# Performance work log

Measured on AMD Instinct MI355X. Metric: run time of the kernel, lower is better.

The kernel has to match this reference:

```python
import jax, jax.numpy as jnp
import numpy as np
import math

B, S, D = 1, 2048, 2048
H, HD, KV = 16, 128, 1
E, F, TOPK = 8, 4096, 2
EPS = 1e-5


def setup_inputs() -> dict:
    key = jax.random.key(0)
    ks = jax.random.split(key, 14)
    sc = 0.02
    inp = {
        "x": jax.random.normal(ks[0], (B, S, D), dtype=jnp.float32),
        "wq": jax.random.normal(ks[1], (D, H * HD), dtype=jnp.float32) * sc,
        "wk": jax.random.normal(ks[2], (D, KV * HD), dtype=jnp.float32) * sc,
        "wv": jax.random.normal(ks[3], (D, KV * HD), dtype=jnp.float32) * sc,
        "wo": jax.random.normal(ks[4], (H * HD, D), dtype=jnp.float32) * sc,
        "w_router": jax.random.normal(ks[5], (D, E), dtype=jnp.float32) * sc,
        "w1": jax.random.normal(ks[6], (E, D, F), dtype=jnp.float32) * sc,
        "w3": jax.random.normal(ks[7], (E, D, F), dtype=jnp.float32) * sc,
        "w2": jax.random.normal(ks[8], (E, F, D), dtype=jnp.float32) * sc,
        "s_pre_mqa": jnp.ones((D,), dtype=jnp.float32),
        "s_post_mqa": jnp.ones((D,), dtype=jnp.float32),
        "s_pre_moe": jnp.ones((D,), dtype=jnp.float32),
        "s_post_moe": jnp.ones((D,), dtype=jnp.float32),
    }
    return inp


def _rmsnorm(x, scale):
    ms = jnp.mean(x * x, axis=-1, keepdims=True)
    return x * jax.lax.rsqrt(ms + EPS) * scale


def _mqa(h, wq, wk, wv, wo):
    b, s, _ = h.shape
    q = (h @ wq).reshape(b, s, H, HD)
    k = (h @ wk).reshape(b, s, KV, HD)
    v = (h @ wv).reshape(b, s, KV, HD)
    # repeat_interleave kv heads up to H (MQA)
    k = jnp.repeat(k, H // KV, axis=2)
    v = jnp.repeat(v, H // KV, axis=2)
    scale = 1.0 / math.sqrt(HD)
    scores = jnp.einsum("bqhd,bkhd->bhqk", q, k) * scale  # [B,H,S,S]
    causal = jnp.tril(jnp.ones((s, s), dtype=bool))
    scores = jnp.where(causal, scores, jnp.float32(-jnp.inf))
    attn = jax.nn.softmax(scores, axis=-1)
    out = jnp.einsum("bhqk,bkhd->bqhd", attn, v).reshape(b, s, H * HD)
    return out @ wo


def _moe(h, w_router, w1, w2, w3):
    logits = h @ w_router                        # [B,S,E]
    probs = jax.nn.softmax(logits, axis=-1)
    topv, topi = jax.lax.top_k(probs, TOPK)      # [B,S,K]
    topv = topv / jnp.sum(topv, axis=-1, keepdims=True)
    # combine weights per expert: [B,S,E]
    combine = jnp.sum(jax.nn.one_hot(topi, E, dtype=h.dtype) * topv[..., None], axis=-2)
    out = jnp.zeros_like(h)
    for e in range(E):  # fixed small expert count
        ye = (jax.nn.silu(h @ w1[e]) * (h @ w3[e])) @ w2[e]
        out = out + combine[..., e:e + 1] * ye
    return out, combine


def reference(x, wq, wk, wv, wo, w_router, w1, w2, w3,
              s_pre_mqa, s_post_mqa, s_pre_moe, s_post_moe):
    mqa_out = _mqa(_rmsnorm(x, s_pre_mqa), wq, wk, wv, wo)
    x = x + _rmsnorm(mqa_out, s_post_mqa)  # dropout p=0 (eval)
    moe_out, router_mask = _moe(_rmsnorm(x, s_pre_moe), w_router, w1, w2, w3)
    x = x + _rmsnorm(moe_out, s_post_moe)
    return x, router_mask
```

## Files before the change

### kernel.cpp

```cpp
#include <hip/hip_runtime.h>

#define S_LEN 2048
#define DM 2048
#define NHEAD 16
#define HDIM 128
#define NEXP 8
#define FF 4096
#define EPSV 1e-5f

typedef unsigned short u16;
typedef short bf16x8 __attribute__((ext_vector_type(8)));
typedef float f32x4 __attribute__((ext_vector_type(4)));

__device__ __forceinline__ f32x4 mfma16(bf16x8 a, bf16x8 b, f32x4 c) {
  return __builtin_amdgcn_mfma_f32_16x16x32_bf16(a, b, c, 0, 0, 0);
}

__device__ __forceinline__ float bf2f(u16 u) {
  union { unsigned int i; float f; } v; v.i = ((unsigned int)u) << 16; return v.f;
}
__device__ __forceinline__ u16 f2bf(float f) {
  union { float f; unsigned int i; } v; v.f = f;
  unsigned int u = v.i;
  return (u16)((u + 0x7fffu + ((u >> 16) & 1u)) >> 16);
}

__device__ __forceinline__ void gload_lds16(const u16* g, u16* l) {
  __builtin_amdgcn_global_load_lds(
      (const __attribute__((address_space(1))) unsigned int*)(unsigned long long)g,
      (__attribute__((address_space(3))) unsigned int*)(unsigned long long)l, 16, 0, 0);
}

__device__ __forceinline__ float blocksum(float v, float* sh) {
#pragma unroll
  for (int off = 32; off; off >>= 1) v += __shfl_xor(v, off, 64);
  const int w = threadIdx.x >> 6;
  if ((threadIdx.x & 63) == 0) sh[w] = v;
  __syncthreads();
  v = sh[0] + sh[1] + sh[2] + sh[3];
  __syncthreads();
  return v;
}

__device__ __forceinline__ void convsplit_body(char* lds, const float* __restrict__ src,
                                               int ld, u16* __restrict__ dhi,
                                               u16* __restrict__ dlo, int nblk, int kblk) {
  float(*tile)[65] = reinterpret_cast<float(*)[65]>(lds);
  const int n0 = nblk * 64, k0 = kblk * 64;
  const int t = threadIdx.x;
  {
    int r = t >> 4, c4 = (t & 15) * 4;
#pragma unroll
    for (int i = 0; i < 4; ++i) {
      float4 v = *reinterpret_cast<const float4*>(src + (size_t)(k0 + r + i * 16) * ld + n0 + c4);
      tile[r + i * 16][c4 + 0] = v.x;
      tile[r + i * 16][c4 + 1] = v.y;
      tile[r + i * 16][c4 + 2] = v.z;
      tile[r + i * 16][c4 + 3] = v.w;
    }
  }
  __syncthreads();
#pragma unroll
  for (int i = 0; i < 2; ++i) {
    int idx = i * 256 + t;
    int n = idx >> 3, kc = (idx & 7) * 8;
    bf16x8 hi, lo;
#pragma unroll
    for (int j = 0; j < 8; ++j) {
      float f = tile[kc + j][n];
      u16 hv = f2bf(f);
      hi[j] = (short)hv;
      lo[j] = (short)f2bf(f - bf2f(hv));
    }
    size_t o = (size_t)(n0 + n) * 2048 + k0 + kc;
    *reinterpret_cast<bf16x8*>(dhi + o) = hi;
    *reinterpret_cast<bf16x8*>(dlo + o) = lo;
  }
}

__device__ __forceinline__ void convT_body(char* lds, const float* __restrict__ src,
                                           int R, int C, u16* __restrict__ dst,
                                           int nblk, int rblk, int e) {
  float(*tile)[65] = reinterpret_cast<float(*)[65]>(lds);
  const int n0 = nblk * 64, r0 = rblk * 64;
  const size_t bofs = (size_t)e * R * C;
  const int t = threadIdx.x;
  {
    int r = t >> 4, c4 = (t & 15) * 4;
#pragma unroll
    for (int i = 0; i < 4; ++i) {
      float4 v = *reinterpret_cast<const float4*>(src + bofs + (size_t)(r0 + r + i * 16) * C + n0 + c4);
      tile[r + i * 16][c4 + 0] = v.x;
      tile[r + i * 16][c4 + 1] = v.y;
      tile[r + i * 16][c4 + 2] = v.z;
      tile[r + i * 16][c4 + 3] = v.w;
    }
  }
  __syncthreads();
#pragma unroll
  for (int i = 0; i < 2; ++i) {
    int idx = i * 256 + t;
    int n = idx >> 3, kc = (idx & 7) * 8;
    bf16x8 pk;
#pragma unroll
    for (int j = 0; j < 8; ++j) pk[j] = (short)f2bf(tile[kc + j][n]);
    *reinterpret_cast<bf16x8*>(dst + bofs + (size_t)(n0 + n) * R + r0 + kc) = pk;
  }
}

__device__ __forceinline__ void convT_body512(char* lds, const float* __restrict__ src,
                                              int R, int C, u16* __restrict__ dst,
                                              int nblk, int rblk, int e) {
  float(*tile)[65] = reinterpret_cast<float(*)[65]>(lds);
  const int n0 = nblk * 64, r0 = rblk * 64;
  const size_t bofs = (size_t)e * R * C;
  const int t = threadIdx.x;
#pragma unroll
  for (int i = 0; i < 2; ++i) {
    int p = i * 512 + t;
    int r = p >> 4, c4 = (p & 15) * 4;
    float4 v = *reinterpret_cast<const float4*>(src + bofs + (size_t)(r0 + r) * C + n0 + c4);
    tile[r][c4 + 0] = v.x;
    tile[r][c4 + 1] = v.y;
    tile[r][c4 + 2] = v.z;
    tile[r][c4 + 3] = v.w;
  }
  __syncthreads();
  {
    int n = t >> 3, kc = (t & 7) * 8;
    bf16x8 pk;
#pragma unroll
    for (int j = 0; j < 8; ++j) pk[j] = (short)f2bf(tile[kc + j][n]);
    *reinterpret_cast<bf16x8*>(dst + bofs + (size_t)(n0 + n) * R + r0 + kc) = pk;
  }
}

__device__ __forceinline__ void rms_pre_body(char* lds, const float* __restrict__ x,
                                             const float* __restrict__ s,
                                             u16* __restrict__ h1, int row) {
  float* sh = (float*)lds;
  const int t = threadIdx.x;
  const float* xr = x + (size_t)row * DM + t * 8;
  float4 a = *reinterpret_cast<const float4*>(xr);
  float4 b = *reinterpret_cast<const float4*>(xr + 4);
  float v[8] = {a.x, a.y, a.z, a.w, b.x, b.y, b.z, b.w};
  float ss = 0.f;
#pragma unroll
  for (int j = 0; j < 8; ++j) ss += v[j] * v[j];
  float inv = rsqrtf(blocksum(ss, sh) * (1.f / DM) + EPSV);
  const float* sp = s + t * 8;
  bf16x8 hi, lo;
#pragma unroll
  for (int j = 0; j < 8; ++j) {
    float val = v[j] * inv * sp[j];
    u16 hv = f2bf(val);
    hi[j] = (short)hv;
    lo[j] = (short)f2bf(val - bf2f(hv));
  }
  *reinterpret_cast<bf16x8*>(h1 + (size_t)row * 4096 + t * 8) = hi;
  *reinterpret_cast<bf16x8*>(h1 + (size_t)row * 4096 + 2048 + t * 8) = lo;
}

__global__ __launch_bounds__(256) void fat_pre(
    const float* __restrict__ x, const float* __restrict__ spre, u16* __restrict__ h1,
    const float* __restrict__ wq, const float* __restrict__ wk, const float* __restrict__ wv,
    u16* __restrict__ BtqHi, u16* __restrict__ BtqLo) {
  __shared__ alignas(16) char lds[16640];
  int bid = blockIdx.x;
  if (bid < 2048) {
    rms_pre_body(lds, x, spre, h1, bid);
  } else if (bid < 3072) {
    int c = bid - 2048;
    convsplit_body(lds, wq, 2048, BtqHi, BtqLo, c & 31, c >> 5);
  } else if (bid < 3136) {
    int c = bid - 3072;
    convsplit_body(lds, wk, 128, BtqHi + (size_t)2048 * 2048, BtqLo + (size_t)2048 * 2048,
                   c & 1, c >> 1);
  } else {
    int c = bid - 3136;
    convsplit_body(lds, wv, 128, BtqHi + (size_t)2176 * 2048, BtqLo + (size_t)2176 * 2048,
                   c & 1, c >> 1);
  }
}

__device__ __forceinline__ void gemm3_body(
    char* lds, const u16* __restrict__ A, const u16* __restrict__ Bthi,
    const u16* __restrict__ Btlo, void* __restrict__ out,
    int mblk, int nblk, int mode, int ldc, int lo_off) {
  const int m0 = mblk * 128, n0 = nblk * 64;
  const int t = threadIdx.x, lane = t & 63, w = t >> 6;
  const int wm = (w >> 1) * 64, wn = (w & 1) * 32;
  const int l15 = lane & 15, lg = lane >> 4;
  const int wbase = t & ~63;

  u16* Ah = (u16*)lds;
  u16* Al = (u16*)(lds + 16384);
  u16* Bh = (u16*)(lds + 32768);
  u16* Bl = (u16*)(lds + 40960);

  const u16* Abh = A + (size_t)m0 * 4096;
  const u16* Abl = Abh + 2048;
  const u16* Bbh = Bthi + (size_t)n0 * 2048;
  const u16* Bbl = Btlo + (size_t)n0 * 2048;

  f32x4 acc[4][2];
#pragma unroll
  for (int m = 0; m < 4; ++m)
#pragma unroll
    for (int n = 0; n < 2; ++n) acc[m][n] = (f32x4){0.f, 0.f, 0.f, 0.f};

  for (int k0 = 0; k0 < 2048; k0 += 64) {
    __syncthreads();
#pragma unroll
    for (int i = 0; i < 4; ++i) {
      int p = i * 256 + t;
      int row = p >> 3;
      int csrc = (p & 7) ^ (row & 7);
      gload_lds16(Abh + (size_t)row * 4096 + k0 + csrc * 8, Ah + (i * 256 + wbase) * 8);
      gload_lds16(Abl + (size_t)row * 4096 + k0 + csrc * 8, Al + (i * 256 + wbase) * 8);
    }
#pragma unroll
    for (int i = 0; i < 2; ++i) {
      int p = i * 256 + t;
      int row = p >> 3;
      int csrc = (p & 7) ^ (row & 7);
      gload_lds16(Bbh + (size_t)row * 2048 + k0 + csrc * 8, Bh + (i * 256 + wbase) * 8);
      gload_lds16(Bbl + (size_t)row * 2048 + k0 + csrc * 8, Bl + (i * 256 + wbase) * 8);
    }
    __syncthreads();
#pragma unroll
    for (int kk = 0; kk < 2; ++kk) {
      bf16x8 ah[4], al[4], bh[2], bl[2];
#pragma unroll
      for (int m = 0; m < 4; ++m) {
        int row = wm + m * 16 + l15;
        int byte = row * 128 + (((kk * 4 + lg) * 16) ^ ((row & 7) << 4));
        ah[m] = *reinterpret_cast<const bf16x8*>((const char*)Ah + byte);
        al[m] = *reinterpret_cast<const bf16x8*>((const char*)Al + byte);
      }
#pragma unroll
      for (int n = 0; n < 2; ++n) {
        int row = wn + n * 16 + l15;
        int byte = row * 128 + (((kk * 4 + lg) * 16) ^ ((row & 7) << 4));
        bh[n] = *reinterpret_cast<const bf16x8*>((const char*)Bh + byte);
        bl[n] = *reinterpret_cast<const bf16x8*>((const char*)Bl + byte);
      }
#pragma unroll
      for (int m = 0; m < 4; ++m)
#pragma unroll
        for (int n = 0; n < 2; ++n) {
          acc[m][n] = mfma16(ah[m], bh[n], acc[m][n]);
          acc[m][n] = mfma16(al[m], bh[n], acc[m][n]);
          acc[m][n] = mfma16(ah[m], bl[n], acc[m][n]);
        }
    }
  }
#pragma unroll
  for (int m = 0; m < 4; ++m)
#pragma unroll
    for (int n = 0; n < 2; ++n)
#pragma unroll
      for (int r = 0; r < 4; ++r) {
        int row = m0 + wm + m * 16 + lg * 4 + r;
        int col = n0 + wn + n * 16 + l15;
        float v = acc[m][n][r];
        if (mode == 1) {
          u16* C = (u16*)out;
          u16 hv = f2bf(v);
          C[(size_t)row * ldc + col] = hv;
          C[(size_t)row * ldc + lo_off + col] = f2bf(v - bf2f(hv));
        } else {
          ((float*)out)[(size_t)row * ldc + col] = v;
        }
      }
}

__global__ __launch_bounds__(256) void gemm3_kernel(
    const u16* __restrict__ A, const u16* __restrict__ Bthi, const u16* __restrict__ Btlo,
    float* __restrict__ out) {
  __shared__ alignas(16) char lds[49152];
  gemm3_body(lds, A, Bthi, Btlo, out, blockIdx.x, blockIdx.y, 2, 2048, 0);
}

__global__ __launch_bounds__(256) void fat_qkv_conv(
    const u16* __restrict__ A, const u16* __restrict__ Bthi, const u16* __restrict__ Btlo,
    u16* __restrict__ QKV, const float* __restrict__ w1, u16* __restrict__ w1t,
    const float* __restrict__ wo, u16* __restrict__ BtoHi, u16* __restrict__ BtoLo) {
  __shared__ alignas(16) char lds[49152];
  int bid = blockIdx.x;
  if (bid < 576) {
    gemm3_body(lds, A, Bthi, Btlo, QKV, bid % 16, bid / 16, 1, 4608, 2304);
  } else {
    int cid = bid - 576;
    if (cid < 16384)
      convT_body(lds, w1, 2048, 4096, w1t, cid % 64, (cid / 64) % 32, cid / 2048);
    else {
      cid -= 16384;
      convsplit_body(lds, wo, 2048, BtoHi, BtoLo, cid & 31, cid >> 5);
    }
  }
}

__global__ __launch_bounds__(256) void vtrans_kernel(const u16* __restrict__ QKV,
                                                     u16* __restrict__ vt) {
  __shared__ u16 tile[64][65];
  const int s0 = blockIdx.x * 64, c0 = blockIdx.y * 64;
  const int t = threadIdx.x;
#pragma unroll
  for (int i = 0; i < 16; ++i) {
    int idx = i * 256 + t;
    int r = idx >> 6, c = idx & 63;
    int col = c0 + c;
    int src = (col < 128) ? (2176 + col) : (4480 + col - 128);
    tile[r][c] = QKV[(size_t)(s0 + r) * 4608 + src];
  }
  __syncthreads();
#pragma unroll
  for (int i = 0; i < 16; ++i) {
    int idx = i * 256 + t;
    int cc = idx >> 6, ss = idx & 63;
    vt[(size_t)(c0 + cc) * S_LEN + s0 + ss] = tile[ss][cc];
  }
}

__device__ __forceinline__ void attn_body(char* lds, const u16* __restrict__ QKV,
                                          const u16* __restrict__ vt, u16* __restrict__ Os,
                                          int bx, int h) {
  const int qb = 31 - bx;
  const int t = threadIdx.x, w = t >> 6, lane = t & 63;
  const int l15 = lane & 15, lg = lane >> 4;
  const int qr0 = qb * 64 + w * 16;
  const int qrow = qr0 + l15;

  u16* Ks = (u16*)lds;
  u16* Vs = (u16*)(lds + 17408);
  u16* myP = (u16*)(lds + 37888) + w * (16 * 72);

  bf16x8 qf[2][4];
#pragma unroll
  for (int p = 0; p < 2; ++p)
#pragma unroll
    for (int c = 0; c < 4; ++c)
      qf[p][c] = *reinterpret_cast<const bf16x8*>(QKV + (size_t)qrow * 4608 + p * 2304 +
                                                  h * 128 + c * 32 + lg * 8);

  f32x4 o[8];
#pragma unroll
  for (int n = 0; n < 8; ++n) o[n] = (f32x4){0.f, 0.f, 0.f, 0.f};
  f32x4 lracc = (f32x4){0.f, 0.f, 0.f, 0.f};
  bf16x8 onesf;
#pragma unroll
  for (int j = 0; j < 8; ++j) onesf[j] = (short)0x3F80;

  const float scale = 0.08838834764831845f;
  const int kend = qb * 64 + 64;

  for (int j0 = 0; j0 < kend; j0 += 32) {
    __syncthreads();
#pragma unroll
    for (int i = 0; i < 4; ++i) {
      int idx = i * 256 + t;
      int row = idx >> 5, seg = idx & 31;
      int srccol = (seg < 16) ? (2048 + seg * 8) : (4352 + (seg - 16) * 8);
      bf16x8 v = *reinterpret_cast<const bf16x8*>(QKV + (size_t)(j0 + row) * 4608 + srccol);
      *reinterpret_cast<bf16x8*>(&Ks[row * 272 + seg * 8]) = v;
    }
#pragma unroll
    for (int i = 0; i < 4; ++i) {
      int idx = i * 256 + t;
      int row = idx >> 2, seg = idx & 3;
      bf16x8 v = *reinterpret_cast<const bf16x8*>(vt + (size_t)row * S_LEN + j0 + seg * 8);
      *reinterpret_cast<bf16x8*>(&Vs[row * 40 + seg * 8]) = v;
    }
    __syncthreads();

    if (j0 > qr0 + 15) continue;
    f32x4 sc[2];
#pragma unroll
    for (int half = 0; half < 2; ++half) {
      const int kb = (half * 16 + l15) * 272;
      f32x4 a0 = (f32x4){0.f, 0.f, 0.f, 0.f};
      f32x4 a1 = (f32x4){0.f, 0.f, 0.f, 0.f};
      f32x4 a2 = (f32x4){0.f, 0.f, 0.f, 0.f};
#pragma unroll
      for (int cc = 0; cc < 4; ++cc) {
        bf16x8 kh = *reinterpret_cast<const bf16x8*>(&Ks[kb + cc * 32 + lg * 8]);
        a0 = mfma16(qf[0][cc], kh, a0);
        a1 = mfma16(qf[1][cc], kh, a1);
      }
#pragma unroll
      for (int cc = 0; cc < 4; ++cc) {
        bf16x8 kl = *reinterpret_cast<const bf16x8*>(&Ks[kb + 128 + cc * 32 + lg * 8]);
        a2 = mfma16(qf[0][cc], kl, a2);
      }
      f32x4 a = (a0 + a1) + a2;
#pragma unroll
      for (int r = 0; r < 4; ++r) {
        int rowg = qr0 + lg * 4 + r;
        int colg = j0 + half * 16 + l15;
        sc[half][r] = (colg <= rowg) ? a[r] * scale : -1e30f;
      }
    }
#pragma unroll
    for (int r = 0; r < 4; ++r) {
      float p0 = __expf(sc[0][r]);
      float p1 = __expf(sc[1][r]);
      int lrow = lg * 4 + r;
      u16 h0 = f2bf(p0), h1v = f2bf(p1);
      myP[lrow * 72 + l15] = h0;
      myP[lrow * 72 + 16 + l15] = h1v;
      myP[lrow * 72 + 32 + l15] = f2bf(p0 - bf2f(h0));
      myP[lrow * 72 + 48 + l15] = f2bf(p1 - bf2f(h1v));
    }
    bf16x8 pfh = *reinterpret_cast<const bf16x8*>(myP + l15 * 72 + lg * 8);
    bf16x8 pfl = *reinterpret_cast<const bf16x8*>(myP + l15 * 72 + 32 + lg * 8);

    lracc = mfma16(pfh, onesf, lracc);
    lracc = mfma16(pfl, onesf, lracc);

#pragma unroll
    for (int n = 0; n < 8; ++n) {
      bf16x8 vh = *reinterpret_cast<const bf16x8*>(&Vs[(n * 16 + l15) * 40 + lg * 8]);
      bf16x8 vl = *reinterpret_cast<const bf16x8*>(&Vs[(n * 16 + l15 + 128) * 40 + lg * 8]);
      o[n] = mfma16(pfh, vh, o[n]);
      o[n] = mfma16(pfl, vh, o[n]);
      o[n] = mfma16(pfh, vl, o[n]);
    }
  }
#pragma unroll
  for (int n = 0; n < 8; ++n)
#pragma unroll
    for (int r = 0; r < 4; ++r) {
      int rowg = qr0 + lg * 4 + r;
      float v = o[n][r] / lracc[r];
      u16 hv = f2bf(v);
      Os[(size_t)rowg * 4096 + h * 128 + n * 16 + l15] = hv;
      Os[(size_t)rowg * 4096 + 2048 + h * 128 + n * 16 + l15] = f2bf(v - bf2f(hv));
    }
}

__global__ __launch_bounds__(256) void fat_attn_conv(
    const u16* __restrict__ QKV, const u16* __restrict__ vt, u16* __restrict__ Os,
    const float* __restrict__ w3, u16* __restrict__ w3t) {
  __shared__ alignas(16) char lds[47104];
  int bid = blockIdx.x;
  if (bid < 512) {
    attn_body(lds, QKV, vt, Os, bid & 31, bid >> 5);
  } else {
    int cid = bid - 512;
    convT_body(lds, w3, 2048, 4096, w3t, cid % 64, (cid / 64) % 32, cid / 2048);
  }
}

__global__ __launch_bounds__(256) void rms_mid_router(
    const float* __restrict__ x, const float* __restrict__ mqa,
    const float* __restrict__ spost, const float* __restrict__ spre,
    const float* __restrict__ wr, float* __restrict__ x1, u16* __restrict__ h2b,
    float* __restrict__ comb, int* __restrict__ topi, float* __restrict__ topw,
    int* __restrict__ cnt) {
  __shared__ float sh1[4];
  __shared__ float sh2[4];
  __shared__ float red[4][8];
  __shared__ float lgits[8];
  const int row = blockIdx.x, t = threadIdx.x;
  const size_t base = (size_t)row * DM + t * 8;
  float mv[8];
  {
    float4 a0 = *reinterpret_cast<const float4*>(mqa + base);
    float4 b0 = *reinterpret_cast<const float4*>(mqa + base + 4);
    mv[0] = a0.x; mv[1] = a0.y; mv[2] = a0.z; mv[3] = a0.w;
    mv[4] = b0.x; mv[5] = b0.y; mv[6] = b0.z; mv[7] = b0.w;
  }
  float ss1 = 0.f;
#pragma unroll
  for (int j = 0; j < 8; ++j) ss1 += mv[j] * mv[j];
  float inv1 = rsqrtf(blocksum(ss1, sh1) * (1.f / DM) + EPSV);
  float4 xa = *reinterpret_cast<const float4*>(x + base);
  float4 xb = *reinterpret_cast<const float4*>(x + base + 4);
  float xv[8] = {xa.x, xa.y, xa.z, xa.w, xb.x, xb.y, xb.z, xb.w};
  float x1v[8];
  float ss2 = 0.f;
#pragma unroll
  for (int j = 0; j < 8; ++j) {
    x1v[j] = xv[j] + mv[j] * inv1 * spost[t * 8 + j];
    ss2 += x1v[j] * x1v[j];
  }
  float inv2 = rsqrtf(blocksum(ss2, sh2) * (1.f / DM) + EPSV);
  *reinterpret_cast<float4*>(x1 + base) = make_float4(x1v[0], x1v[1], x1v[2], x1v[3]);
  *reinterpret_cast<float4*>(x1 + base + 4) = make_float4(x1v[4], x1v[5], x1v[6], x1v[7]);
  float hv[8];
  bf16x8 hb;
#pragma unroll
  for (int j = 0; j < 8; ++j) {
    hv[j] = x1v[j] * inv2 * spre[t * 8 + j];
    hb[j] = (short)f2bf(hv[j]);
  }
  *reinterpret_cast<bf16x8*>(h2b + base) = hb;

  float acc[8] = {0.f, 0.f, 0.f, 0.f, 0.f, 0.f, 0.f, 0.f};
  const float* wrow = wr + (size_t)t * 64;
#pragma unroll
  for (int j = 0; j < 8; ++j) {
    const float* wj = wrow + j * 8;
#pragma unroll
    for (int e = 0; e < 8; ++e) acc[e] += hv[j] * wj[e];
  }
#pragma unroll
  for (int off = 32; off; off >>= 1)
#pragma unroll
    for (int e = 0; e < 8; ++e) acc[e] += __shfl_xor(acc[e], off, 64);
  const int w = t >> 6;
  if ((t & 63) == 0) {
#pragma unroll
    for (int e = 0; e < 8; ++e) red[w][e] = acc[e];
  }
  __syncthreads();
  if (t < 8) lgits[t] = red[0][t] + red[1][t] + red[2][t] + red[3][t];
  __syncthreads();
  if (t == 0) {
    float L[8], mx = -1e30f;
#pragma unroll
    for (int e = 0; e < 8; ++e) {
      L[e] = lgits[e];
      mx = fmaxf(mx, L[e]);
    }
    float p[8], s = 0.f;
#pragma unroll
    for (int e = 0; e < 8; ++e) {
      p[e] = expf(L[e] - mx);
      s += p[e];
    }
#pragma unroll
    for (int e = 0; e < 8; ++e) p[e] /= s;
    int e0 = 0;
    for (int e = 1; e < 8; ++e)
      if (p[e] > p[e0]) e0 = e;
    int e1 = (e0 == 0) ? 1 : 0;
    for (int e = 0; e < 8; ++e)
      if (e != e0 && p[e] > p[e1]) e1 = e;
    float ssum = p[e0] + p[e1];
    float w0 = p[e0] / ssum, w1 = p[e1] / ssum;
    for (int e = 0; e < 8; ++e)
      comb[(size_t)row * 8 + e] = (e == e0) ? w0 : ((e == e1) ? w1 : 0.f);
    topi[2 * row] = e0;
    topi[2 * row + 1] = e1;
    topw[2 * row] = w0;
    topw[2 * row + 1] = w1;
    atomicAdd(&cnt[e0], 1);
    atomicAdd(&cnt[e1], 1);
  }
}

__global__ void zero_meta_kernel(int* __restrict__ cnt) {
  if (threadIdx.x < NEXP) cnt[threadIdx.x] = 0;
}

__global__ void build_meta_kernel(const int* __restrict__ cnt, int* __restrict__ cursor,
                                  int* __restrict__ meta) {
  if (threadIdx.x != 0) return;
  int off = 0, nt = 0;
  for (int e = 0; e < NEXP; ++e) {
    int c = cnt[e];
    cursor[e] = off;
    int ntl = (c + 255) >> 8;
    for (int r = 0; r < ntl; ++r) {
      meta[8 + nt] = e;
      meta[64 + nt] = off + r * 256;
      int rem = c - r * 256;
      meta[120 + nt] = rem < 256 ? rem : 256;
      ++nt;
    }
    off += c;
  }
  meta[0] = nt;
}

__global__ void scatter_kernel(const int* __restrict__ topi, int* __restrict__ cursor,
                               int* __restrict__ ptok, int* __restrict__ pos_of) {
  int token = blockIdx.x * 256 + threadIdx.x;
  if (token >= S_LEN) return;
  for (int k = 0; k < 2; ++k) {
    int e = topi[2 * token + k];
    int pos = atomicAdd(&cursor[e], 1);
    ptok[pos] = token;
    pos_of[2 * token + k] = pos;
  }
}

__device__ __forceinline__ void moe_gemm1_body(
    u16* As, u16* B1s, u16* B3s, int* toks,
    const u16* __restrict__ H2, const u16* __restrict__ W1t, const u16* __restrict__ W3t,
    u16* __restrict__ U, const int* __restrict__ meta, const int* __restrict__ ptok,
    int tile, int n0blk) {
  if (tile >= meta[0]) return;
  const int e = meta[8 + tile], row0 = meta[64 + tile], rows = meta[120 + tile];
  const int n0 = n0blk * 64;
  const u16* B1 = W1t + (size_t)e * FF * DM + (size_t)n0 * 2048;
  const u16* B3 = W3t + (size_t)e * FF * DM + (size_t)n0 * 2048;
  const int t = threadIdx.x, lane = t & 63, w = t >> 6;
  const int wm = (w >> 1) * 64, wn = (w & 1) * 32;
  const int l15 = lane & 15, lg = lane >> 4;
  const int wbase = t & ~63;

  if (t < 256) toks[t] = (t < rows) ? ptok[row0 + t] : ptok[row0];
  __syncthreads();

  f32x4 aG[4][2], aT[4][2];
#pragma unroll
  for (int m = 0; m < 4; ++m)
#pragma unroll
    for (int n = 0; n < 2; ++n) {
      aG[m][n] = (f32x4){0.f, 0.f, 0.f, 0.f};
      aT[m][n] = (f32x4){0.f, 0.f, 0.f, 0.f};
    }

  for (int k0 = 0; k0 < DM; k0 += 64) {
    __syncthreads();
#pragma unroll
    for (int i = 0; i < 4; ++i) {
      int p = i * 512 + t;
      int row = p >> 3;
      int csrc = (p & 7) ^ (row & 7);
      gload_lds16(H2 + (size_t)toks[row] * DM + k0 + csrc * 8, As + (i * 512 + wbase) * 8);
    }
    {
      int row = t >> 3;
      int csrc = (t & 7) ^ (row & 7);
      gload_lds16(B1 + (size_t)row * 2048 + k0 + csrc * 8, B1s + wbase * 8);
      gload_lds16(B3 + (size_t)row * 2048 + k0 + csrc * 8, B3s + wbase * 8);
    }
    __syncthreads();
#pragma unroll
    for (int kk = 0; kk < 2; ++kk) {
      bf16x8 af[4], b1f[2], b3f[2];
#pragma unroll
      for (int m = 0; m < 4; ++m) {
        int row = wm + m * 16 + l15;
        int byte = row * 128 + (((kk * 4 + lg) * 16) ^ ((row & 7) << 4));
        af[m] = *reinterpret_cast<const bf16x8*>((const char*)As + byte);
      }
#pragma unroll
      for (int n = 0; n < 2; ++n) {
        int row = wn + n * 16 + l15;
        int byte = row * 128 + (((kk * 4 + lg) * 16) ^ ((row & 7) << 4));
        b1f[n] = *reinterpret_cast<const bf16x8*>((const char*)B1s + byte);
        b3f[n] = *reinterpret_cast<const bf16x8*>((const char*)B3s + byte);
      }
#pragma unroll
      for (int m = 0; m < 4; ++m)
#pragma unroll
        for (int n = 0; n < 2; ++n) {
          aG[m][n] = mfma16(af[m], b1f[n], aG[m][n]);
          aT[m][n] = mfma16(af[m], b3f[n], aT[m][n]);
        }
    }
  }
#pragma unroll
  for (int m = 0; m < 4; ++m)
#pragma unroll
    for (int n = 0; n < 2; ++n)
#pragma unroll
      for (int r = 0; r < 4; ++r) {
        int lrow = wm + m * 16 + lg * 4 + r;
        if (lrow < rows) {
          float g = aG[m][n][r], tt = aT[m][n][r];
          float u = (g / (1.f + __expf(-g))) * tt;
          U[(size_t)(row0 + lrow) * FF + n0 + wn + n * 16 + l15] = f2bf(u);
        }
      }
}

__global__ __launch_bounds__(512) void fat_moe1(
    const u16* __restrict__ H2, const u16* __restrict__ W1t, const u16* __restrict__ W3t,
    u16* __restrict__ U, const int* __restrict__ meta, const int* __restrict__ ptok,
    const float* __restrict__ w2, u16* __restrict__ w2t) {
  __shared__ alignas(16) u16 As[16384];
  __shared__ alignas(16) u16 B1s[4096];
  __shared__ alignas(16) u16 B3s[4096];
  __shared__ int toks[256];
  int bid = blockIdx.x;
  if (bid < 1536) {
    moe_gemm1_body(As, B1s, B3s, toks, H2, W1t, W3t, U, meta, ptok, bid % 24, bid / 24);
  } else {
    int cid = bid - 1536;
    convT_body512((char*)As, w2, 4096, 2048, w2t, cid % 32, (cid / 32) % 64, cid / 2048);
  }
}

__global__ __launch_bounds__(512) void moe_gemm2b(
    const u16* __restrict__ U, const u16* __restrict__ W2t, u16* __restrict__ Y,
    const int* __restrict__ meta) {
  const int tile = blockIdx.x;
  if (tile >= meta[0]) return;
  const int e = meta[8 + tile], row0 = meta[64 + tile], rows = meta[120 + tile];
  const int n0 = blockIdx.y * 128;
  const u16* Bb = W2t + (size_t)e * DM * FF + (size_t)n0 * 4096;
  const int t = threadIdx.x, lane = t & 63, w = t >> 6;
  const int wm = (w >> 1) * 64, wn = (w & 1) * 64;
  const int l15 = lane & 15, lg = lane >> 4;
  const int wbase = t & ~63;

  __shared__ alignas(16) u16 As[16384];
  __shared__ alignas(16) u16 Bs[8192];

  f32x4 acc[4][4];
#pragma unroll
  for (int m = 0; m < 4; ++m)
#pragma unroll
    for (int n = 0; n < 4; ++n) acc[m][n] = (f32x4){0.f, 0.f, 0.f, 0.f};

  for (int k0 = 0; k0 < FF; k0 += 64) {
    __syncthreads();
#pragma unroll
    for (int i = 0; i < 4; ++i) {
      int p = i * 512 + t;
      int row = p >> 3;
      int csrc = (p & 7) ^ (row & 7);
      gload_lds16(U + (size_t)(row0 + row) * FF + k0 + csrc * 8, As + (i * 512 + wbase) * 8);
    }
#pragma unroll
    for (int i = 0; i < 2; ++i) {
      int p = i * 512 + t;
      int row = p >> 3;
      int csrc = (p & 7) ^ (row & 7);
      gload_lds16(Bb + (size_t)row * 4096 + k0 + csrc * 8, Bs + (i * 512 + wbase) * 8);
    }
    __syncthreads();
#pragma unroll
    for (int kk = 0; kk < 2; ++kk) {
      bf16x8 af[4], bfr[4];
#pragma unroll
      for (int m = 0; m < 4; ++m) {
        int row = wm + m * 16 + l15;
        int byte = row * 128 + (((kk * 4 + lg) * 16) ^ ((row & 7) << 4));
        af[m] = *reinterpret_cast<const bf16x8*>((const char*)As + byte);
      }
#pragma unroll
      for (int n = 0; n < 4; ++n) {
        int row = wn + n * 16 + l15;
        int byte = row * 128 + (((kk * 4 + lg) * 16) ^ ((row & 7) << 4));
        bfr[n] = *reinterpret_cast<const bf16x8*>((const char*)Bs + byte);
      }
#pragma unroll
      for (int m = 0; m < 4; ++m)
#pragma unroll
        for (int n = 0; n < 4; ++n) acc[m][n] = mfma16(af[m], bfr[n], acc[m][n]);
    }
  }
#pragma unroll
  for (int m = 0; m < 4; ++m)
#pragma unroll
    for (int n = 0; n < 4; ++n)
#pragma unroll
      for (int r = 0; r < 4; ++r) {
        int lrow = wm + m * 16 + lg * 4 + r;
        if (lrow < rows)
          Y[(size_t)(row0 + lrow) * DM + n0 + wn + n * 16 + l15] = f2bf(acc[m][n][r]);
      }
}

__global__ __launch_bounds__(256) void moe_final_kernel(
    const float* __restrict__ x1, const u16* __restrict__ Y,
    const int* __restrict__ pos_of, const float* __restrict__ topw,
    const float* __restrict__ spost, float* __restrict__ xout) {
  __shared__ float sh[4];
  const int row = blockIdx.x, t = threadIdx.x;
  const int p0 = pos_of[2 * row], p1 = pos_of[2 * row + 1];
  const float w0 = topw[2 * row], w1 = topw[2 * row + 1];
  bf16x8 y0 = *reinterpret_cast<const bf16x8*>(Y + (size_t)p0 * DM + t * 8);
  bf16x8 y1 = *reinterpret_cast<const bf16x8*>(Y + (size_t)p1 * DM + t * 8);
  float mv[8];
  float ss = 0.f;
#pragma unroll
  for (int j = 0; j < 8; ++j) {
    mv[j] = w0 * bf2f((u16)y0[j]) + w1 * bf2f((u16)y1[j]);
    ss += mv[j] * mv[j];
  }
  float inv = rsqrtf(blocksum(ss, sh) * (1.f / DM) + EPSV);
  const size_t base = (size_t)row * DM + t * 8;
#pragma unroll
  for (int j = 0; j < 8; ++j)
    xout[base + j] = x1[base + j] + mv[j] * inv * spost[t * 8 + j];
}

extern "C" void kernel_launch(void* const* d_in, const int* in_sizes, int n_in,
                              void* d_out, int out_size, void* d_ws, size_t ws_size,
                              hipStream_t stream) {
  (void)in_sizes; (void)n_in; (void)out_size; (void)ws_size;
  const float* x = (const float*)d_in[0];
  const float* wq = (const float*)d_in[1];
  const float* wk = (const float*)d_in[2];
  const float* wv = (const float*)d_in[3];
  const float* wo = (const float*)d_in[4];
  const float* wrt = (const float*)d_in[5];
  const float* w1 = (const float*)d_in[6];
  const float* w3 = (const float*)d_in[7];
  const float* w2 = (const float*)d_in[8];
  const float* s_pre_mqa = (const float*)d_in[9];
  const float* s_post_mqa = (const float*)d_in[10];
  const float* s_pre_moe = (const float*)d_in[11];
  const float* s_post_moe = (const float*)d_in[12];

  float* xout = (float*)d_out;
  float* out_router = xout + (size_t)S_LEN * DM;

  char* wsp = (char*)d_ws;
  size_t off = 0;
  auto alloc = [&](size_t n) {
    char* p = wsp + off;
    off += (n + 255) & ~(size_t)255;
    return p;
  };
  u16* U = (u16*)alloc((size_t)4096 * FF * 2);
  u16* Y = (u16*)alloc((size_t)4096 * DM * 2);
  float* mqa = (float*)alloc((size_t)S_LEN * DM * 4);
  u16* h1s = (u16*)alloc((size_t)S_LEN * 4096 * 2);
  u16* attn_s = h1s;
  u16* Btq_hi = (u16*)alloc((size_t)2304 * 2048 * 2);
  u16* Btq_lo = (u16*)alloc((size_t)2304 * 2048 * 2);
  u16* Bto_hi = (u16*)alloc((size_t)2048 * 2048 * 2);
  u16* Bto_lo = (u16*)alloc((size_t)2048 * 2048 * 2);
  u16* QKV = (u16*)alloc((size_t)S_LEN * 4608 * 2);
  u16* vt = (u16*)alloc((size_t)256 * S_LEN * 2);
  float* x1 = (float*)alloc((size_t)S_LEN * DM * 4);
  u16* h2b = (u16*)alloc((size_t)S_LEN * DM * 2);
  int* topi = (int*)alloc(4096 * 4);
  float* topw = (float*)alloc(4096 * 4);
  int* pos_of = (int*)alloc(4096 * 4);
  int* ptok = (int*)alloc(4352 * 4);
  int* cnt = (int*)alloc(32 * 4);
  int* cursor = (int*)alloc(32 * 4);
  int* meta = (int*)alloc(256 * 4);
  u16* w1t = (u16*)alloc((size_t)NEXP * DM * FF * 2);
  u16* w3t = (u16*)alloc((size_t)NEXP * DM * FF * 2);
  u16* w2t = (u16*)alloc((size_t)NEXP * FF * DM * 2);

  dim3 B256(256);
  dim3 B512(512);

  fat_pre<<<dim3(3200), B256, 0, stream>>>(x, s_pre_mqa, h1s, wq, wk, wv, Btq_hi, Btq_lo);
  fat_qkv_conv<<<dim3(576 + 16384 + 1024), B256, 0, stream>>>(
      h1s, Btq_hi, Btq_lo, QKV, w1, w1t, wo, Bto_hi, Bto_lo);
  vtrans_kernel<<<dim3(32, 4), B256, 0, stream>>>(QKV, vt);
  fat_attn_conv<<<dim3(512 + 16384), B256, 0, stream>>>(QKV, vt, attn_s, w3, w3t);
  gemm3_kernel<<<dim3(16, 32), B256, 0, stream>>>(attn_s, Bto_hi, Bto_lo, mqa);
  zero_meta_kernel<<<dim3(1), dim3(64), 0, stream>>>(cnt);
  rms_mid_router<<<dim3(S_LEN), B256, 0, stream>>>(x, mqa, s_post_mqa, s_pre_moe, wrt,
                                                   x1, h2b, out_router, topi, topw, cnt);
  build_meta_kernel<<<dim3(1), dim3(64), 0, stream>>>(cnt, cursor, meta);
  scatter_kernel<<<dim3(8), B256, 0, stream>>>(topi, cursor, ptok, pos_of);
  fat_moe1<<<dim3(1536 + 16384), B512, 0, stream>>>(h2b, w1t, w3t, U, meta, ptok, w2, w2t);
  moe_gemm2b<<<dim3(24, 16), B512, 0, stream>>>(U, w2t, Y, meta);
  moe_final_kernel<<<dim3(S_LEN), B256, 0, stream>>>(x1, Y, pos_of, topw, s_post_moe, xout);
}
```

Baseline: 817.4 us.

## Shrink MoE gemm1 tiles to 128 rows and co-schedule w2 conversion with Wo GEMM

Half of the w2 weight transpose/conversion (experts 0-3) is moved into a new fused kernel that runs alongside the Wo output-projection GEMM. The rest stays co-scheduled with MoE gemm1. MoE gemm1 now uses 128-row token tiles from a second metadata table, with 8 waves each computing 64x16. This gives more blocks and less padding, in exchange for lower per-block reuse of the weight tiles. The aim is to fill idle CUs during the small Wo GEMM and balance the MoE up-projection launch.

```diff
diff --git a/kernel.cpp b/kernel.cpp
--- a/kernel.cpp
+++ b/kernel.cpp
@@ -275,13 +275,6 @@
       }
 }
 
-__global__ __launch_bounds__(256) void gemm3_kernel(
-    const u16* __restrict__ A, const u16* __restrict__ Bthi, const u16* __restrict__ Btlo,
-    float* __restrict__ out) {
-  __shared__ alignas(16) char lds[49152];
-  gemm3_body(lds, A, Bthi, Btlo, out, blockIdx.x, blockIdx.y, 2, 2048, 0);
-}
-
 __global__ __launch_bounds__(256) void fat_qkv_conv(
     const u16* __restrict__ A, const u16* __restrict__ Bthi, const u16* __restrict__ Btlo,
     u16* __restrict__ QKV, const float* __restrict__ w1, u16* __restrict__ w1t,
@@ -449,6 +442,19 @@
   } else {
     int cid = bid - 512;
     convT_body(lds, w3, 2048, 4096, w3t, cid % 64, (cid / 64) % 32, cid / 2048);
+  }
+}
+
+__global__ __launch_bounds__(256) void fat_wo_conv(
+    const u16* __restrict__ A, const u16* __restrict__ Bthi, const u16* __restrict__ Btlo,
+    float* __restrict__ out, const float* __restrict__ w2, u16* __restrict__ w2t) {
+  __shared__ alignas(16) char lds[49152];
+  int bid = blockIdx.x;
+  if (bid < 512) {
+    gemm3_body(lds, A, Bthi, Btlo, out, bid & 15, bid >> 4, 2, 2048, 0);
+  } else {
+    int cid = bid - 512;
+    convT_body(lds, w2, 4096, 2048, w2t, cid % 32, (cid / 32) % 64, cid / 2048);
   }
 }
 
@@ -556,9 +562,9 @@
 }
 
 __global__ void build_meta_kernel(const int* __restrict__ cnt, int* __restrict__ cursor,
-                                  int* __restrict__ meta) {
+                                  int* __restrict__ meta, int* __restrict__ meta128) {
   if (threadIdx.x != 0) return;
-  int off = 0, nt = 0;
+  int off = 0, nt = 0, nt2 = 0;
   for (int e = 0; e < NEXP; ++e) {
     int c = cnt[e];
     cursor[e] = off;
@@ -570,9 +576,18 @@
       meta[120 + nt] = rem < 256 ? rem : 256;
       ++nt;
     }
+    int ntl2 = (c + 127) >> 7;
+    for (int r = 0; r < ntl2; ++r) {
+      meta128[8 + nt2] = e;
+      meta128[64 + nt2] = off + r * 128;
+      int rem = c - r * 128;
+      meta128[120 + nt2] = rem < 128 ? rem : 128;
+      ++nt2;
+    }
     off += c;
   }
   meta[0] = nt;
+  meta128[0] = nt2;
 }
 
 __global__ void scatter_kernel(const int* __restrict__ topi, int* __restrict__ cursor,
@@ -588,36 +603,37 @@
 }
 
 __device__ __forceinline__ void moe_gemm1_body(
-    u16* As, u16* B1s, u16* B3s, int* toks,
-    const u16* __restrict__ H2, const u16* __restrict__ W1t, const u16* __restrict__ W3t,
-    u16* __restrict__ U, const int* __restrict__ meta, const int* __restrict__ ptok,
-    int tile, int n0blk) {
+    char* lds, const u16* __restrict__ H2, const u16* __restrict__ W1t,
+    const u16* __restrict__ W3t, u16* __restrict__ U, const int* __restrict__ meta,
+    const int* __restrict__ ptok, int tile, int n0blk) {
   if (tile >= meta[0]) return;
+  u16* As = (u16*)lds;
+  u16* B1s = (u16*)(lds + 16384);
+  u16* B3s = (u16*)(lds + 24576);
+  int* toks = (int*)(lds + 32768);
   const int e = meta[8 + tile], row0 = meta[64 + tile], rows = meta[120 + tile];
   const int n0 = n0blk * 64;
   const u16* B1 = W1t + (size_t)e * FF * DM + (size_t)n0 * 2048;
   const u16* B3 = W3t + (size_t)e * FF * DM + (size_t)n0 * 2048;
   const int t = threadIdx.x, lane = t & 63, w = t >> 6;
-  const int wm = (w >> 1) * 64, wn = (w & 1) * 32;
+  const int wm = (w >> 2) * 64, wn = (w & 3) * 16;
   const int l15 = lane & 15, lg = lane >> 4;
   const int wbase = t & ~63;
 
-  if (t < 256) toks[t] = (t < rows) ? ptok[row0 + t] : ptok[row0];
+  if (t < 128) toks[t] = (t < rows) ? ptok[row0 + t] : ptok[row0];
   __syncthreads();
 
-  f32x4 aG[4][2], aT[4][2];
-#pragma unroll
-  for (int m = 0; m < 4; ++m)
-#pragma unroll
-    for (int n = 0; n < 2; ++n) {
-      aG[m][n] = (f32x4){0.f, 0.f, 0.f, 0.f};
-      aT[m][n] = (f32x4){0.f, 0.f, 0.f, 0.f};
-    }
+  f32x4 aG[4], aT[4];
+#pragma unroll
+  for (int m = 0; m < 4; ++m) {
+    aG[m] = (f32x4){0.f, 0.f, 0.f, 0.f};
+    aT[m] = (f32x4){0.f, 0.f, 0.f, 0.f};
+  }
 
   for (int k0 = 0; k0 < DM; k0 += 64) {
     __syncthreads();
 #pragma unroll
-    for (int i = 0; i < 4; ++i) {
+    for (int i = 0; i < 2; ++i) {
       int p = i * 512 + t;
       int row = p >> 3;
       int csrc = (p & 7) ^ (row & 7);
@@ -632,58 +648,50 @@
     __syncthreads();
 #pragma unroll
     for (int kk = 0; kk < 2; ++kk) {
-      bf16x8 af[4], b1f[2], b3f[2];
+      bf16x8 af[4], b1f, b3f;
 #pragma unroll
       for (int m = 0; m < 4; ++m) {
         int row = wm + m * 16 + l15;
         int byte = row * 128 + (((kk * 4 + lg) * 16) ^ ((row & 7) << 4));
         af[m] = *reinterpret_cast<const bf16x8*>((const char*)As + byte);
       }
-#pragma unroll
-      for (int n = 0; n < 2; ++n) {
-        int row = wn + n * 16 + l15;
+      {
+        int row = wn + l15;
         int byte = row * 128 + (((kk * 4 + lg) * 16) ^ ((row & 7) << 4));
-        b1f[n] = *reinterpret_cast<const bf16x8*>((const char*)B1s + byte);
-        b3f[n] = *reinterpret_cast<const bf16x8*>((const char*)B3s + byte);
-      }
-#pragma unroll
-      for (int m = 0; m < 4; ++m)
-#pragma unroll
-        for (int n = 0; n < 2; ++n) {
-          aG[m][n] = mfma16(af[m], b1f[n], aG[m][n]);
-          aT[m][n] = mfma16(af[m], b3f[n], aT[m][n]);
-        }
+        b1f = *reinterpret_cast<const bf16x8*>((const char*)B1s + byte);
+        b3f = *reinterpret_cast<const bf16x8*>((const char*)B3s + byte);
+      }
+#pragma unroll
+      for (int m = 0; m < 4; ++m) {
+        aG[m] = mfma16(af[m], b1f, aG[m]);
+        aT[m] = mfma16(af[m], b3f, aT[m]);
+      }
     }
   }
 #pragma unroll
   for (int m = 0; m < 4; ++m)
 #pragma unroll
-    for (int n = 0; n < 2; ++n)
-#pragma unroll
-      for (int r = 0; r < 4; ++r) {
-        int lrow = wm + m * 16 + lg * 4 + r;
-        if (lrow < rows) {
-          float g = aG[m][n][r], tt = aT[m][n][r];
-          float u = (g / (1.f + __expf(-g))) * tt;
-          U[(size_t)(row0 + lrow) * FF + n0 + wn + n * 16 + l15] = f2bf(u);
-        }
-      }
+    for (int r = 0; r < 4; ++r) {
+      int lrow = wm + m * 16 + lg * 4 + r;
+      if (lrow < rows) {
+        float g = aG[m][r], tt = aT[m][r];
+        float u = (g / (1.f + __expf(-g))) * tt;
+        U[(size_t)(row0 + lrow) * FF + n0 + wn + l15] = f2bf(u);
+      }
+    }
 }
 
 __global__ __launch_bounds__(512) void fat_moe1(
     const u16* __restrict__ H2, const u16* __restrict__ W1t, const u16* __restrict__ W3t,
-    u16* __restrict__ U, const int* __restrict__ meta, const int* __restrict__ ptok,
+    u16* __restrict__ U, const int* __restrict__ meta128, const int* __restrict__ ptok,
     const float* __restrict__ w2, u16* __restrict__ w2t) {
-  __shared__ alignas(16) u16 As[16384];
-  __shared__ alignas(16) u16 B1s[4096];
-  __shared__ alignas(16) u16 B3s[4096];
-  __shared__ int toks[256];
+  __shared__ alignas(16) char lds[33280];
   int bid = blockIdx.x;
-  if (bid < 1536) {
-    moe_gemm1_body(As, B1s, B3s, toks, H2, W1t, W3t, U, meta, ptok, bid % 24, bid / 24);
+  if (bid < 2560) {
+    moe_gemm1_body(lds, H2, W1t, W3t, U, meta128, ptok, bid >> 6, bid & 63);
   } else {
-    int cid = bid - 1536;
-    convT_body512((char*)As, w2, 4096, 2048, w2t, cid % 32, (cid / 32) % 64, cid / 2048);
+    int cid = bid - 2560;
+    convT_body512(lds, w2, 4096, 2048, w2t, cid % 32, (cid / 32) % 64, 4 + cid / 2048);
   }
 }
 
@@ -831,6 +839,7 @@
   int* cnt = (int*)alloc(32 * 4);
   int* cursor = (int*)alloc(32 * 4);
   int* meta = (int*)alloc(256 * 4);
+  int* meta128 = (int*)alloc(256 * 4);
   u16* w1t = (u16*)alloc((size_t)NEXP * DM * FF * 2);
   u16* w3t = (u16*)alloc((size_t)NEXP * DM * FF * 2);
   u16* w2t = (u16*)alloc((size_t)NEXP * FF * DM * 2);
@@ -843,13 +852,13 @@
       h1s, Btq_hi, Btq_lo, QKV, w1, w1t, wo, Bto_hi, Bto_lo);
   vtrans_kernel<<<dim3(32, 4), B256, 0, stream>>>(QKV, vt);
   fat_attn_conv<<<dim3(512 + 16384), B256, 0, stream>>>(QKV, vt, attn_s, w3, w3t);
-  gemm3_kernel<<<dim3(16, 32), B256, 0, stream>>>(attn_s, Bto_hi, Bto_lo, mqa);
+  fat_wo_conv<<<dim3(512 + 8192), B256, 0, stream>>>(attn_s, Bto_hi, Bto_lo, mqa, w2, w2t);
   zero_meta_kernel<<<dim3(1), dim3(64), 0, stream>>>(cnt);
   rms_mid_router<<<dim3(S_LEN), B256, 0, stream>>>(x, mqa, s_post_mqa, s_pre_moe, wrt,
                                                    x1, h2b, out_router, topi, topw, cnt);
-  build_meta_kernel<<<dim3(1), dim3(64), 0, stream>>>(cnt, cursor, meta);
+  build_meta_kernel<<<dim3(1), dim3(64), 0, stream>>>(cnt, cursor, meta, meta128);
   scatter_kernel<<<dim3(8), B256, 0, stream>>>(topi, cursor, ptok, pos_of);
-  fat_moe1<<<dim3(1536 + 16384), B512, 0, stream>>>(h2b, w1t, w3t, U, meta, ptok, w2, w2t);
+  fat_moe1<<<dim3(2560 + 8192), B512, 0, stream>>>(h2b, w1t, w3t, U, meta128, ptok, w2, w2t);
   moe_gemm2b<<<dim3(24, 16), B512, 0, stream>>>(U, w2t, Y, meta);
   moe_final_kernel<<<dim3(S_LEN), B256, 0, stream>>>(x1, Y, pos_of, topw, s_post_moe, xout);
 }
```

Measured after the change: 781.0 us. 4.5% less time.
